# Kernel tuning notes

Hardware: AMD Instinct MI355X
Metric: run time of the kernel (lower is better)

The kernel has to match this reference:

```python
import jax, jax.numpy as jnp
import numpy as np

ALPHA = 16.0

def setup_inputs() -> dict:
    key = jax.random.key(0)
    k1, k2, k3, k4, k5 = jax.random.split(key, 5)
    B_, S, D_in, D_out, R = 4, 4096, 4096, 4096, 16
    x = jax.random.normal(k1, (B_, S, D_in), dtype=jnp.float32)
    W = jax.random.normal(k2, (D_out, D_in), dtype=jnp.float32) * 0.02
    A = jax.random.normal(k3, (R, D_in), dtype=jnp.float32) * 0.02
    Bm = jax.random.normal(k4, (D_out, R), dtype=jnp.float32) * 0.02
    bias = jax.random.normal(k5, (D_out,), dtype=jnp.float32)
    return {"x": x, "W": W, "A": A, "B": Bm, "bias": bias}

def reference(x, W, A, B, bias):
    # weight = W + (B @ A) * alpha ; out = x @ weight.T + bias
    weight = W + (B @ A) * ALPHA          # [D_out, D_in]
    return jnp.einsum('bsi,oi->bso', x, weight) + bias
```

## Files before the change

kernel.cpp:

```cpp
#include <hip/hip_runtime.h>
#include <hip/hip_bf16.h>

typedef short bf16x8 __attribute__((ext_vector_type(8)));
typedef short s16x4 __attribute__((ext_vector_type(4)));
typedef float f32x4 __attribute__((ext_vector_type(4)));

static constexpr int MTOT = 16384;
static constexpr int NDIM = 4096;
static constexpr int KDIM = 4096;
static constexpr float LORA_ALPHA = 16.0f;

__device__ __forceinline__ unsigned bf16rn_bits(float v) {
  unsigned b = __float_as_uint(v);
  return (b + 0x7FFFu + ((b >> 16) & 1u)) >> 16;
}

__device__ __forceinline__ void split4(const float4 v, s16x4& h, s16x4& l) {
  float f[4] = {v.x, v.y, v.z, v.w};
  #pragma unroll
  for (int e = 0; e < 4; ++e) {
    unsigned hb = bf16rn_bits(f[e]);
    float hf = __uint_as_float(hb << 16);
    float lv = f[e] - hf;
    h[e] = (short)hb;
    l[e] = (short)bf16rn_bits(lv);
  }
}

__global__ __launch_bounds__(256) void lora_T_kernel(
    const float* __restrict__ x, const float* __restrict__ A,
    float* __restrict__ T) {
  const int wave = threadIdx.x >> 6;
  const int lane = threadIdx.x & 63;
  const int m0 = blockIdx.x * 16 + wave * 4;

  float acc[4][16];
  #pragma unroll
  for (int i = 0; i < 4; ++i)
    #pragma unroll
    for (int r = 0; r < 16; ++r) acc[i][r] = 0.f;

  for (int k0 = 0; k0 < KDIM; k0 += 256) {
    const int k = k0 + lane * 4;
    float4 xv[4];
    #pragma unroll
    for (int i = 0; i < 4; ++i)
      xv[i] = *(const float4*)&x[(size_t)(m0 + i) * KDIM + k];
    #pragma unroll
    for (int r = 0; r < 16; ++r) {
      float4 av = *(const float4*)&A[r * KDIM + k];
      #pragma unroll
      for (int i = 0; i < 4; ++i) {
        acc[i][r] += xv[i].x * av.x + xv[i].y * av.y +
                     xv[i].z * av.z + xv[i].w * av.w;
      }
    }
  }

  #pragma unroll
  for (int i = 0; i < 4; ++i)
    #pragma unroll
    for (int r = 0; r < 16; ++r) {
      float v = acc[i][r];
      #pragma unroll
      for (int off = 32; off; off >>= 1) v += __shfl_xor(v, off, 64);
      acc[i][r] = v;
    }

  const int i = lane >> 4, r = lane & 15;
  T[(size_t)(m0 + i) * 16 + r] = acc[i][r];
}

__global__ __launch_bounds__(256, 2) void lora_gemm_kernel(
    const float* __restrict__ x, const float* __restrict__ W,
    const float* __restrict__ Bm, const float* __restrict__ bias,
    const float* __restrict__ T, float* __restrict__ out) {

  __shared__ short smem[4 * 128 * 64];

  const int tid = threadIdx.x;
  const int per = gridDim.x >> 3;
  const int swz = (blockIdx.x & 7) * per + (blockIdx.x >> 3);
  const int bm = swz / (NDIM / 128);
  const int bn = swz % (NDIM / 128);

  const int srow = tid >> 4;
  const int sc4 = tid & 15;
  const float* xg = x + (size_t)(bm * 128 + srow) * KDIM + sc4 * 4;
  const float* wg = W + (size_t)(bn * 128 + srow) * KDIM + sc4 * 4;

  float4 xr[8], wr[8];

  auto loadTile = [&](int kt) {
    const float* xp = xg + kt * 64;
    const float* wp = wg + kt * 64;
    #pragma unroll
    for (int i = 0; i < 8; ++i) {
      xr[i] = *(const float4*)(xp + (size_t)(i * 16) * KDIM);
      wr[i] = *(const float4*)(wp + (size_t)(i * 16) * KDIM);
    }
  };

  auto writeTile = [&]() {
    #pragma unroll
    for (int i = 0; i < 8; ++i) {
      const int row = srow + i * 16;
      const int idx = row * 64 + ((sc4 * 4) ^ ((row & 7) << 3));
      s16x4 h, l;
      split4(xr[i], h, l);
      *(s16x4*)&smem[idx] = h;
      *(s16x4*)&smem[8192 + idx] = l;
      split4(wr[i], h, l);
      *(s16x4*)&smem[16384 + idx] = h;
      *(s16x4*)&smem[24576 + idx] = l;
    }
  };

  const int lane = tid & 63;
  const int wave = tid >> 6;
  const int wm = wave >> 1, wn = wave & 1;
  const int frow = lane & 15;
  const int fk = (lane >> 4) * 8;

  f32x4 acc[4][4];
  #pragma unroll
  for (int i = 0; i < 4; ++i)
    #pragma unroll
    for (int j = 0; j < 4; ++j) acc[i][j] = (f32x4){0.f, 0.f, 0.f, 0.f};

  loadTile(0);
  constexpr int NT = KDIM / 64;
  for (int kt = 0; kt < NT; ++kt) {
    __syncthreads();
    writeTile();
    __syncthreads();
    if (kt + 1 < NT) loadTile(kt + 1);

    #pragma unroll
    for (int kk = 0; kk < 2; ++kk) {
      const int colk = kk * 32 + fk;
      bf16x8 ah[4], al[4], bh[4], bl[4];
      #pragma unroll
      for (int t = 0; t < 4; ++t) {
        const int ra = wm * 64 + t * 16 + frow;
        const int ia = ra * 64 + (colk ^ ((ra & 7) << 3));
        ah[t] = *(const bf16x8*)&smem[ia];
        al[t] = *(const bf16x8*)&smem[8192 + ia];
        const int rb = wn * 64 + t * 16 + frow;
        const int ib = rb * 64 + (colk ^ ((rb & 7) << 3));
        bh[t] = *(const bf16x8*)&smem[16384 + ib];
        bl[t] = *(const bf16x8*)&smem[24576 + ib];
      }
      #pragma unroll
      for (int mt = 0; mt < 4; ++mt)
        #pragma unroll
        for (int nt = 0; nt < 4; ++nt) {
          acc[mt][nt] = __builtin_amdgcn_mfma_f32_16x16x32_bf16(ah[mt], bh[nt], acc[mt][nt], 0, 0, 0);
          acc[mt][nt] = __builtin_amdgcn_mfma_f32_16x16x32_bf16(al[mt], bh[nt], acc[mt][nt], 0, 0, 0);
          acc[mt][nt] = __builtin_amdgcn_mfma_f32_16x16x32_bf16(ah[mt], bl[nt], acc[mt][nt], 0, 0, 0);
        }
    }
  }

  const int m0 = bm * 128 + wm * 64;
  const int n0 = bn * 128 + wn * 64;

  float4 brow[4][4];
  float bs[4];
  #pragma unroll
  for (int nt = 0; nt < 4; ++nt) {
    const int n = n0 + nt * 16 + frow;
    #pragma unroll
    for (int q = 0; q < 4; ++q)
      brow[nt][q] = *(const float4*)&Bm[n * 16 + q * 4];
    bs[nt] = bias[n];
  }

  const int rbase = (lane >> 4) * 4;
  #pragma unroll
  for (int mt = 0; mt < 4; ++mt) {
    #pragma unroll
    for (int r = 0; r < 4; ++r) {
      const int m = m0 + mt * 16 + rbase + r;
      float4 t4[4];
      #pragma unroll
      for (int q = 0; q < 4; ++q)
        t4[q] = *(const float4*)&T[(size_t)m * 16 + q * 4];
      #pragma unroll
      for (int nt = 0; nt < 4; ++nt) {
        float corr =
            t4[0].x * brow[nt][0].x + t4[0].y * brow[nt][0].y + t4[0].z * brow[nt][0].z + t4[0].w * brow[nt][0].w +
            t4[1].x * brow[nt][1].x + t4[1].y * brow[nt][1].y + t4[1].z * brow[nt][1].z + t4[1].w * brow[nt][1].w +
            t4[2].x * brow[nt][2].x + t4[2].y * brow[nt][2].y + t4[2].z * brow[nt][2].z + t4[2].w * brow[nt][2].w +
            t4[3].x * brow[nt][3].x + t4[3].y * brow[nt][3].y + t4[3].z * brow[nt][3].z + t4[3].w * brow[nt][3].w;
        out[(size_t)m * NDIM + n0 + nt * 16 + frow] =
            acc[mt][nt][r] + bs[nt] + LORA_ALPHA * corr;
      }
    }
  }
}

extern "C" void kernel_launch(void* const* d_in, const int* in_sizes, int n_in,
                              void* d_out, int out_size, void* d_ws, size_t ws_size,
                              hipStream_t stream) {
  const float* x    = (const float*)d_in[0];
  const float* W    = (const float*)d_in[1];
  const float* A    = (const float*)d_in[2];
  const float* Bm   = (const float*)d_in[3];
  const float* bias = (const float*)d_in[4];
  float* out = (float*)d_out;
  float* T   = (float*)d_ws;

  hipLaunchKernelGGL(lora_T_kernel, dim3(MTOT / 16), dim3(256), 0, stream,
                     x, A, T);
  hipLaunchKernelGGL(lora_gemm_kernel,
                     dim3((MTOT / 128) * (NDIM / 128)), dim3(256), 0, stream,
                     x, W, Bm, bias, T, out);
}
```

Baseline: 2.440 ms.

## Pre-split x and W into tiled bf16 hi/lo buffers, load via global_load_lds

```diff
diff --git a/kernel.cpp b/kernel.cpp
--- a/kernel.cpp
+++ b/kernel.cpp
@@ -8,7 +8,15 @@
 static constexpr int MTOT = 16384;
 static constexpr int NDIM = 4096;
 static constexpr int KDIM = 4096;
+static constexpr int NKT  = KDIM / 64;
 static constexpr float LORA_ALPHA = 16.0f;
+
+static constexpr size_t OFF_AXH = 0;
+static constexpr size_t OFF_AXL = OFF_AXH + (size_t)MTOT * KDIM * 2;
+static constexpr size_t OFF_WH  = OFF_AXL + (size_t)MTOT * KDIM * 2;
+static constexpr size_t OFF_WL  = OFF_WH  + (size_t)NDIM * KDIM * 2;
+static constexpr size_t OFF_T   = OFF_WL  + (size_t)NDIM * KDIM * 2;
+static constexpr size_t WS_NEED = OFF_T + (size_t)MTOT * 16 * 4;
 
 __device__ __forceinline__ unsigned bf16rn_bits(float v) {
   unsigned b = __float_as_uint(v);
@@ -27,6 +35,34 @@
   }
 }
 
+typedef __attribute__((address_space(3))) unsigned int lds_u32;
+typedef __attribute__((address_space(1))) const unsigned int glb_u32;
+__device__ __forceinline__ void gl2lds16(const short* g, short* l) {
+  __builtin_amdgcn_global_load_lds((glb_u32*)g, (lds_u32*)l, 16, 0, 0);
+}
+
+__global__ __launch_bounds__(256) void convert_split_kernel(
+    const float* __restrict__ src, short* __restrict__ dh,
+    short* __restrict__ dl) {
+  const size_t e = (size_t)blockIdx.x * 256 + threadIdx.x;
+  const int m  = (int)(e >> 9);
+  const int c8 = (int)(e & 511);
+  const int k  = c8 << 3;
+  const float* p = src + ((size_t)m << 12) + k;
+  float4 v0 = *(const float4*)p;
+  float4 v1 = *(const float4*)(p + 4);
+  s16x4 h0, l0, h1, l1;
+  split4(v0, h0, l0);
+  split4(v1, h1, l1);
+  const int rtile = m >> 7, row = m & 127, ktile = k >> 6, kin = k & 63;
+  const size_t base = ((size_t)rtile * NKT + ktile) * 8192;
+  const int idx = row * 64 + (kin ^ ((row & 7) << 3));
+  bf16x8 h = {h0[0], h0[1], h0[2], h0[3], h1[0], h1[1], h1[2], h1[3]};
+  bf16x8 l = {l0[0], l0[1], l0[2], l0[3], l1[0], l1[1], l1[2], l1[3]};
+  *(bf16x8*)&dh[base + idx] = h;
+  *(bf16x8*)&dl[base + idx] = l;
+}
+
 __global__ __launch_bounds__(256) void lora_T_kernel(
     const float* __restrict__ x, const float* __restrict__ A,
     float* __restrict__ T) {
@@ -71,7 +107,134 @@
   T[(size_t)(m0 + i) * 16 + r] = acc[i][r];
 }
 
-__global__ __launch_bounds__(256, 2) void lora_gemm_kernel(
+__global__ __launch_bounds__(512, 4) void lora_gemm_pre(
+    const short* __restrict__ Axh, const short* __restrict__ Axl,
+    const short* __restrict__ Wh,  const short* __restrict__ Wl,
+    const float* __restrict__ Bm,  const float* __restrict__ bias,
+    const float* __restrict__ T,   float* __restrict__ out) {
+
+  __shared__ short smem[4 * 128 * 64];
+  short* const sxh = smem;
+  short* const sxl = smem + 8192;
+  short* const swh = smem + 16384;
+  short* const swl = smem + 24576;
+
+  const int tid = threadIdx.x;
+  const int per = gridDim.x >> 3;
+  const int swz = (blockIdx.x & 7) * per + (blockIdx.x >> 3);
+  const int bm = swz / (NDIM / 128);
+  const int bn = swz % (NDIM / 128);
+
+  const short* baseAh = Axh + ((size_t)bm * NKT) * 8192;
+  const short* baseAl = Axl + ((size_t)bm * NKT) * 8192;
+  const short* baseWh = Wh + ((size_t)bn * NKT) * 8192;
+  const short* baseWl = Wl + ((size_t)bn * NKT) * 8192;
+
+  const int lane = tid & 63;
+  const int wave = tid >> 6;
+  const int wm = wave >> 2, wn = wave & 3;
+  const int frow = lane & 15;
+  const int fk = (lane >> 4) * 8;
+
+  f32x4 acc[4][2];
+  #pragma unroll
+  for (int i = 0; i < 4; ++i)
+    #pragma unroll
+    for (int j = 0; j < 2; ++j) acc[i][j] = (f32x4){0.f, 0.f, 0.f, 0.f};
+
+  const int soff0 = tid * 8;
+  const int soff1 = soff0 + 4096;
+
+  for (int kt = 0; kt < NKT; ++kt) {
+    __syncthreads();
+    {
+      const size_t tb = (size_t)kt * 8192;
+      gl2lds16(baseAh + tb + soff0, sxh + soff0);
+      gl2lds16(baseAh + tb + soff1, sxh + soff1);
+      gl2lds16(baseAl + tb + soff0, sxl + soff0);
+      gl2lds16(baseAl + tb + soff1, sxl + soff1);
+      gl2lds16(baseWh + tb + soff0, swh + soff0);
+      gl2lds16(baseWh + tb + soff1, swh + soff1);
+      gl2lds16(baseWl + tb + soff0, swl + soff0);
+      gl2lds16(baseWl + tb + soff1, swl + soff1);
+    }
+    __syncthreads();
+
+    #pragma unroll
+    for (int kk = 0; kk < 2; ++kk) {
+      const int colk = kk * 32 + fk;
+      bf16x8 ah[4], al[4], bh[2], bl[2];
+      #pragma unroll
+      for (int mt = 0; mt < 4; ++mt) {
+        const int ra = wm * 64 + mt * 16 + frow;
+        const int ia = ra * 64 + (colk ^ ((ra & 7) << 3));
+        ah[mt] = *(const bf16x8*)&sxh[ia];
+        al[mt] = *(const bf16x8*)&sxl[ia];
+      }
+      #pragma unroll
+      for (int nt = 0; nt < 2; ++nt) {
+        const int rb = wn * 32 + nt * 16 + frow;
+        const int ib = rb * 64 + (colk ^ ((rb & 7) << 3));
+        bh[nt] = *(const bf16x8*)&swh[ib];
+        bl[nt] = *(const bf16x8*)&swl[ib];
+      }
+      #pragma unroll
+      for (int mt = 0; mt < 4; ++mt)
+        #pragma unroll
+        for (int nt = 0; nt < 2; ++nt)
+          acc[mt][nt] = __builtin_amdgcn_mfma_f32_16x16x32_bf16(ah[mt], bh[nt], acc[mt][nt], 0, 0, 0);
+      #pragma unroll
+      for (int mt = 0; mt < 4; ++mt)
+        #pragma unroll
+        for (int nt = 0; nt < 2; ++nt)
+          acc[mt][nt] = __builtin_amdgcn_mfma_f32_16x16x32_bf16(al[mt], bh[nt], acc[mt][nt], 0, 0, 0);
+      #pragma unroll
+      for (int mt = 0; mt < 4; ++mt)
+        #pragma unroll
+        for (int nt = 0; nt < 2; ++nt)
+          acc[mt][nt] = __builtin_amdgcn_mfma_f32_16x16x32_bf16(ah[mt], bl[nt], acc[mt][nt], 0, 0, 0);
+    }
+  }
+
+  const int m0 = bm * 128 + wm * 64;
+  const int n0 = bn * 128 + wn * 32;
+
+  float4 brow[2][4];
+  float bs[2];
+  #pragma unroll
+  for (int nt = 0; nt < 2; ++nt) {
+    const int n = n0 + nt * 16 + frow;
+    #pragma unroll
+    for (int q = 0; q < 4; ++q)
+      brow[nt][q] = *(const float4*)&Bm[n * 16 + q * 4];
+    bs[nt] = bias[n];
+  }
+
+  const int rbase = (lane >> 4) * 4;
+  #pragma unroll
+  for (int mt = 0; mt < 4; ++mt) {
+    #pragma unroll
+    for (int r = 0; r < 4; ++r) {
+      const int m = m0 + mt * 16 + rbase + r;
+      float4 t4[4];
+      #pragma unroll
+      for (int q = 0; q < 4; ++q)
+        t4[q] = *(const float4*)&T[(size_t)m * 16 + q * 4];
+      #pragma unroll
+      for (int nt = 0; nt < 2; ++nt) {
+        float corr =
+            t4[0].x * brow[nt][0].x + t4[0].y * brow[nt][0].y + t4[0].z * brow[nt][0].z + t4[0].w * brow[nt][0].w +
+            t4[1].x * brow[nt][1].x + t4[1].y * brow[nt][1].y + t4[1].z * brow[nt][1].z + t4[1].w * brow[nt][1].w +
+            t4[2].x * brow[nt][2].x + t4[2].y * brow[nt][2].y + t4[2].z * brow[nt][2].z + t4[2].w * brow[nt][2].w +
+            t4[3].x * brow[nt][3].x + t4[3].y * brow[nt][3].y + t4[3].z * brow[nt][3].z + t4[3].w * brow[nt][3].w;
+        out[(size_t)m * NDIM + n0 + nt * 16 + frow] =
+            acc[mt][nt][r] + bs[nt] + LORA_ALPHA * corr;
+      }
+    }
+  }
+}
+
+__global__ __launch_bounds__(256, 2) void lora_gemm_fallback(
     const float* __restrict__ x, const float* __restrict__ W,
     const float* __restrict__ Bm, const float* __restrict__ bias,
     const float* __restrict__ T, float* __restrict__ out) {
@@ -209,11 +372,30 @@
   const float* Bm   = (const float*)d_in[3];
   const float* bias = (const float*)d_in[4];
   float* out = (float*)d_out;
-  float* T   = (float*)d_ws;
-
-  hipLaunchKernelGGL(lora_T_kernel, dim3(MTOT / 16), dim3(256), 0, stream,
-                     x, A, T);
-  hipLaunchKernelGGL(lora_gemm_kernel,
-                     dim3((MTOT / 128) * (NDIM / 128)), dim3(256), 0, stream,
-                     x, W, Bm, bias, T, out);
-}
+  char* ws = (char*)d_ws;
+
+  if (ws_size >= WS_NEED) {
+    short* Axh = (short*)(ws + OFF_AXH);
+    short* Axl = (short*)(ws + OFF_AXL);
+    short* Wh  = (short*)(ws + OFF_WH);
+    short* Wl  = (short*)(ws + OFF_WL);
+    float* T   = (float*)(ws + OFF_T);
+
+    hipLaunchKernelGGL(convert_split_kernel, dim3(NDIM * 2), dim3(256), 0,
+                       stream, W, Wh, Wl);
+    hipLaunchKernelGGL(convert_split_kernel, dim3(MTOT * 2), dim3(256), 0,
+                       stream, x, Axh, Axl);
+    hipLaunchKernelGGL(lora_T_kernel, dim3(MTOT / 16), dim3(256), 0, stream,
+                       x, A, T);
+    hipLaunchKernelGGL(lora_gemm_pre,
+                       dim3((MTOT / 128) * (NDIM / 128)), dim3(512), 0, stream,
+                       Axh, Axl, Wh, Wl, Bm, bias, T, out);
+  } else {
+    float* T = (float*)ws;
+    hipLaunchKernelGGL(lora_T_kernel, dim3(MTOT / 16), dim3(256), 0, stream,
+                       x, A, T);
+    hipLaunchKernelGGL(lora_gemm_fallback,
+                       dim3((MTOT / 128) * (NDIM / 128)), dim3(256), 0, stream,
+                       x, W, Bm, bias, T, out);
+  }
+}
```

Result: faster. 1.998 ms (-18.1%).
